# Optimization experiments

Hardware: AMD Instinct MI355X
Metric: run time of the kernel (lower is better)

The kernel has to match this reference:

```python
import jax, jax.numpy as jnp
import numpy as np

B, N, IN_DIM, OUT_DIM, HEADS = 4, 2048, 128, 32, 8
NEG_SLOPE = 0.2


def setup_inputs() -> dict:
    key = jax.random.key(0)
    k_x, k_adj, k_w, k_as, k_ad = jax.random.split(key, 5)
    x = jax.random.normal(k_x, (B, N, IN_DIM), dtype=jnp.float32)
    adj = jax.random.randint(k_adj, (B, N, N), 0, 2).astype(jnp.float32)
    # xavier_uniform bounds
    lim_w = float(np.sqrt(6.0 / (IN_DIM + OUT_DIM)))
    lim_a = float(np.sqrt(6.0 / (OUT_DIM + 1)))
    W = jax.random.uniform(k_w, (HEADS, IN_DIM, OUT_DIM), dtype=jnp.float32, minval=-lim_w, maxval=lim_w)
    a_src = jax.random.uniform(k_as, (HEADS, OUT_DIM), dtype=jnp.float32, minval=-lim_a, maxval=lim_a)
    a_dst = jax.random.uniform(k_ad, (HEADS, OUT_DIM), dtype=jnp.float32, minval=-lim_a, maxval=lim_a)
    return {"x": x, "adj": adj, "W": W, "a_src": a_src, "a_dst": a_dst}


def reference(x, adj, W, a_src, a_dst):
    # Wh: [B,H,N,O]
    Wh = jnp.einsum('bnf,hfo->bhno', x, W)
    alpha_src = jnp.einsum('bhno,ho->bhn', Wh, a_src)  # [B,H,N]
    alpha_dst = jnp.einsum('bhno,ho->bhn', Wh, a_dst)  # [B,H,N]
    # additive scores e[b,h,i,j] = alpha_src[b,h,i] + alpha_dst[b,h,j]
    e = alpha_src[..., :, None] + alpha_dst[..., None, :]
    e = jnp.where(e >= 0, e, NEG_SLOPE * e)  # leaky_relu(0.2)
    n = adj.shape[-1]
    eye = jnp.eye(n, dtype=adj.dtype)
    mask = (adj + eye[None] > 0)[:, None, :, :]  # [B,1,N,N]
    e = jnp.where(mask, e, -jnp.inf)
    attn = jax.nn.softmax(e, axis=-1)  # every row has self-loop -> finite
    out = jnp.einsum('bhij,bhjo->bhio', attn, Wh)  # [B,H,N,O]
    b = x.shape[0]
    out = jnp.transpose(out, (0, 2, 1, 3)).reshape(b, n, HEADS * OUT_DIM)
    return jax.nn.relu(out)
```

## Files before the change

### kernel.cpp

```cpp
#include <hip/hip_runtime.h>
#include <math.h>

#define BB 4
#define NSZ 2048
#define FDIM 128
#define ODIM 32
#define HH 8

typedef short short8 __attribute__((ext_vector_type(8)));
typedef _Float16 half8 __attribute__((ext_vector_type(8)));
typedef float f32x4 __attribute__((ext_vector_type(4)));

#define WS_EAP  0
#define WS_EBP  131072
#define WS_ADJB 262144
#define WS_WHF  786432

__device__ __forceinline__ unsigned hpack(float a, float b) {
    unsigned r;
    asm("v_cvt_pkrtz_f16_f32 %0, %1, %2" : "=v"(r) : "v"(a), "v"(b));
    return r;
}

__global__ __launch_bounds__(256) void k_prep(const float* __restrict__ x,
                                              const float* __restrict__ adj,
                                              const float* __restrict__ W,
                                              const float* __restrict__ a_src,
                                              const float* __restrict__ a_dst,
                                              unsigned* __restrict__ adjb,
                                              int4* __restrict__ whf,
                                              float* __restrict__ eap,
                                              unsigned short* __restrict__ ebe,
                                              unsigned short* __restrict__ ebe2) {
    __shared__ float wsl[FDIM * 33];
    __shared__ unsigned short wlds[64][33];
    int t = threadIdx.x;

    if (blockIdx.x >= 1024) {
        int bid = blockIdx.x - 1024;
#pragma unroll
        for (int it = 0; it < 4; it++) {
            int g = (it * 4096 + bid) * 256 + t;
            int l = g & 7;
            int word = g >> 3;
            int wk = word & 63;
            int row = word >> 6;
            int i = row & (NSZ - 1);
            const float4 v = *(const float4*)&adj[(size_t)row * NSZ + wk * 32 + l * 4];
            unsigned m = 0;
            if (v.x > 0.f) m |= 1u << (l * 4 + 0);
            if (v.y > 0.f) m |= 1u << (l * 4 + 1);
            if (v.z > 0.f) m |= 1u << (l * 4 + 2);
            if (v.w > 0.f) m |= 1u << (l * 4 + 3);
            m |= (unsigned)__shfl_xor((int)m, 1);
            m |= (unsigned)__shfl_xor((int)m, 2);
            m |= (unsigned)__shfl_xor((int)m, 4);
            if (l == 0) {
                int jb = i - wk * 32;
                if (jb >= 0 && jb < 32) m |= 1u << jb;
                adjb[word] = m;
            }
        }
        return;
    }

    int bidx = blockIdx.x;
    int b = bidx >> 8;
    int h = (bidx >> 5) & 7;
    int nt = bidx & 31;
    int n0 = nt * 64;
    int w = t >> 6, lane = t & 63;
    int col = lane & 15, quad = lane >> 4;

#pragma unroll
    for (int m = 0; m < 16; m++) {
        int idx = t + m * 256;
        wsl[(idx >> 5) * 33 + (idx & 31)] = W[(size_t)h * (FDIM * ODIM) + idx];
    }

    const float* xp = x + ((size_t)(b * NSZ) + n0 + w * 16 + col) * FDIM + quad * 8;
    int4 afr[4];
#pragma unroll
    for (int kt = 0; kt < 4; kt++) {
        float4 xa = *(const float4*)(xp + kt * 32);
        float4 xb = *(const float4*)(xp + kt * 32 + 4);
        afr[kt] = make_int4((int)hpack(xa.x, xa.y), (int)hpack(xa.z, xa.w),
                            (int)hpack(xb.x, xb.y), (int)hpack(xb.z, xb.w));
    }
    __syncthreads();

    f32x4 alo = {0.f, 0.f, 0.f, 0.f};
    f32x4 ahi = {0.f, 0.f, 0.f, 0.f};
#pragma unroll
    for (int kt = 0; kt < 4; kt++) {
        half8 a8 = __builtin_bit_cast(half8, afr[kt]);
#pragma unroll
        for (int ot = 0; ot < 2; ot++) {
            unsigned d[4];
#pragma unroll
            for (int jp = 0; jp < 4; jp++) {
                float lo = wsl[(kt * 32 + quad * 8 + 2 * jp) * 33 + ot * 16 + col];
                float hi = wsl[(kt * 32 + quad * 8 + 2 * jp + 1) * 33 + ot * 16 + col];
                d[jp] = hpack(lo, hi);
            }
            int4 bf = make_int4((int)d[0], (int)d[1], (int)d[2], (int)d[3]);
            if (ot == 0)
                alo = __builtin_amdgcn_mfma_f32_16x16x32_f16(a8,
                        __builtin_bit_cast(half8, bf), alo, 0, 0, 0);
            else
                ahi = __builtin_amdgcn_mfma_f32_16x16x32_f16(a8,
                        __builtin_bit_cast(half8, bf), ahi, 0, 0, 0);
        }
    }

    float as0 = a_src[h * ODIM + col], as1 = a_src[h * ODIM + 16 + col];
    float ad0 = a_dst[h * ODIM + col], ad1 = a_dst[h * ODIM + 16 + col];
#pragma unroll
    for (int r = 0; r < 4; r++) {
        float pa = alo[r] * as0 + ahi[r] * as1;
        float pb = alo[r] * ad0 + ahi[r] * ad1;
#pragma unroll
        for (int mk = 1; mk <= 8; mk <<= 1) {
            pa += __shfl_xor(pa, mk);
            pb += __shfl_xor(pb, mk);
        }
        if (col == 0) {
            size_t idx = (size_t)(b * HH + h) * NSZ + n0 + w * 16 + quad * 4 + r;
            eap[idx]  = __expf(-0.8f * pa);
            ebe[idx]  = (unsigned short)(hpack(__expf(pb - 2.f), 0.f) & 0xffffu);
            ebe2[idx] = (unsigned short)(hpack(__expf(0.2f * pb - 2.f), 0.f) & 0xffffu);
        }
    }

#pragma unroll
    for (int r = 0; r < 4; r++) {
        wlds[w * 16 + quad * 4 + r][col]      = (unsigned short)(hpack(alo[r], 0.f) & 0xffffu);
        wlds[w * 16 + quad * 4 + r][col + 16] = (unsigned short)(hpack(ahi[r], 0.f) & 0xffffu);
    }
    __syncthreads();
    int jl = w >> 1, ot = w & 1;
    unsigned d[4];
#pragma unroll
    for (int jp = 0; jp < 4; jp++) {
        unsigned lo = wlds[jl * 32 + quad * 8 + 2 * jp][ot * 16 + col];
        unsigned hi = wlds[jl * 32 + quad * 8 + 2 * jp + 1][ot * 16 + col];
        d[jp] = (hi << 16) | lo;
    }
    int fragid = ((b * HH + h) * 64 + nt * 2 + jl) * 2 + ot;
    whf[(size_t)fragid * 64 + lane] = make_int4((int)d[0], (int)d[1], (int)d[2], (int)d[3]);
}

template<int B>
__device__ __forceinline__ unsigned mexp2(unsigned w, unsigned selhi) {
    unsigned lo, hi, r;
    asm("v_bfe_i32 %0, %1, %2, 1" : "=v"(lo) : "v"(w), "i"(B));
    asm("v_bfe_i32 %0, %1, %2, 1" : "=v"(hi) : "v"(w), "i"(B + 1));
    asm("v_bfi_b32 %0, %1, %2, %3" : "=v"(r) : "s"(selhi), "v"(hi), "v"(lo));
    return r;
}

__device__ __forceinline__ int4 pfrag16(unsigned R2, uint4 e, uint4 g,
                                        unsigned w8, unsigned selhi) {
    unsigned r0, r1, r2, r3, q0, q1, q2, q3;
    asm("v_pk_mul_f16 %0, %1, %2" : "=v"(r0) : "v"(R2), "v"(g.x));
    asm("v_pk_mul_f16 %0, %1, %2" : "=v"(r1) : "v"(R2), "v"(g.y));
    asm("v_pk_mul_f16 %0, %1, %2" : "=v"(r2) : "v"(R2), "v"(g.z));
    asm("v_pk_mul_f16 %0, %1, %2" : "=v"(r3) : "v"(R2), "v"(g.w));
    asm("v_pk_max_f16 %0, %1, %2" : "=v"(q0) : "v"(e.x), "v"(r0));
    asm("v_pk_max_f16 %0, %1, %2" : "=v"(q1) : "v"(e.y), "v"(r1));
    asm("v_pk_max_f16 %0, %1, %2" : "=v"(q2) : "v"(e.z), "v"(r2));
    asm("v_pk_max_f16 %0, %1, %2" : "=v"(q3) : "v"(e.w), "v"(r3));
    return make_int4((int)(q0 & mexp2<0>(w8, selhi)),
                     (int)(q1 & mexp2<2>(w8, selhi)),
                     (int)(q2 & mexp2<4>(w8, selhi)),
                     (int)(q3 & mexp2<6>(w8, selhi)));
}

__global__ __launch_bounds__(256) void k_gat(const int4* __restrict__ whf,
                                             const float* __restrict__ eap,
                                             const unsigned short* __restrict__ ebe,
                                             const unsigned short* __restrict__ ebe2,
                                             const unsigned* __restrict__ adjb,
                                             float* __restrict__ out) {
    __shared__ __align__(16) float smem[2048];
    unsigned short* eble = (unsigned short*)smem;
    unsigned short* eblf = (unsigned short*)smem + 2048;

    int t = threadIdx.x;
    int u = blockIdx.x;
    int unit = (u & 7) * 512 + (u >> 3);
    int b = unit >> 10;
    int h = (unit >> 7) & 7;
    int i0 = (unit & 127) * 16;
    int wave = t >> 6, lane = t & 63;
    int col = lane & 15, quad = lane >> 4, qsh = quad * 8;
    size_t bh = (size_t)(b * HH + h);
    const unsigned selhi = 0xFFFF0000u;

    const float4* ege = (const float4*)(ebe + bh * NSZ);
    const float4* egf = (const float4*)(ebe2 + bh * NSZ);
    ((float4*)eble)[t] = ege[t];
    ((float4*)eblf)[t] = egf[t];

    float R = eap[bh * NSZ + i0 + col];
    unsigned R2 = hpack(R, R);
    const char* mbase = (const char*)(adjb + ((size_t)(b * NSZ) + i0 + col) * 64)
                        + (size_t)wave * 64;
    const int4* bfp = whf + bh * 8192 + (size_t)(wave * 16) * 128 + lane;

    f32x4 a0 = {0.f, 0.f, 0.f, 0.f};
    f32x4 a1 = {0.f, 0.f, 0.f, 0.f};
    f32x4 ad = {0.f, 0.f, 0.f, 0.f};
    const int4 onesv = make_int4(0x3C003C00, 0x3C003C00, 0x3C003C00, 0x3C003C00);
    half8 hones = __builtin_bit_cast(half8, onesv);

    __syncthreads();

    for (int g = 0; g < 4; g++) {
        uint4 m0 = *(const uint4*)(mbase + g * 16);
        int4 blo[4], bhi[4];
#pragma unroll
        for (int q = 0; q < 4; q++) {
            blo[q] = bfp[(g * 4 + q) * 128];
            bhi[q] = bfp[(g * 4 + q) * 128 + 64];
        }
        unsigned ma[4] = {m0.x, m0.y, m0.z, m0.w};
#pragma unroll
        for (int q = 0; q < 4; q++) {
            int jt = wave * 16 + g * 4 + q;
            uint4 ef = *(const uint4*)&eble[jt * 32 + qsh];
            uint4 gf = *(const uint4*)&eblf[jt * 32 + qsh];
            int4 fr = pfrag16(R2, ef, gf, ma[q] >> qsh, selhi);
            half8 af = __builtin_bit_cast(half8, fr);
            half8 b0 = __builtin_bit_cast(half8, blo[q]);
            half8 b1 = __builtin_bit_cast(half8, bhi[q]);
            a0 = __builtin_amdgcn_mfma_f32_16x16x32_f16(af, b0, a0, 0, 0, 0);
            a1 = __builtin_amdgcn_mfma_f32_16x16x32_f16(af, b1, a1, 0, 0, 0);
            ad = __builtin_amdgcn_mfma_f32_16x16x32_f16(af, hones, ad, 0, 0, 0);
        }
    }

    f32x4 (*cb)[3][64] = (f32x4 (*)[3][64])smem;
    __syncthreads();
    if (wave >= 2) {
        cb[wave - 2][0][lane] = a0;
        cb[wave - 2][1][lane] = a1;
        cb[wave - 2][2][lane] = ad;
    }
    __syncthreads();
    if (wave < 2) {
        a0 += cb[wave][0][lane];
        a1 += cb[wave][1][lane];
        ad += cb[wave][2][lane];
    }
    __syncthreads();
    if (wave == 1) {
        cb[0][0][lane] = a0;
        cb[0][1][lane] = a1;
        cb[0][2][lane] = ad;
    }
    __syncthreads();
    if (wave != 0) return;
    a0 += cb[0][0][lane];
    a1 += cb[0][1][lane];
    ad += cb[0][2][lane];

    float* op = out + ((size_t)(b * NSZ) + i0) * (HH * ODIM) + h * ODIM + col;
#pragma unroll
    for (int r = 0; r < 4; r++) {
        int row = quad * 4 + r;
        float inv = 1.0f / ad[r];
        op[(size_t)row * (HH * ODIM)]      = fmaxf(a0[r] * inv, 0.f);
        op[(size_t)row * (HH * ODIM) + 16] = fmaxf(a1[r] * inv, 0.f);
    }
}

extern "C" void kernel_launch(void* const* d_in, const int* in_sizes, int n_in,
                              void* d_out, int out_size, void* d_ws, size_t ws_size,
                              hipStream_t stream) {
    const float* x     = (const float*)d_in[0];
    const float* adj   = (const float*)d_in[1];
    const float* W     = (const float*)d_in[2];
    const float* a_src = (const float*)d_in[3];
    const float* a_dst = (const float*)d_in[4];
    float* out = (float*)d_out;

    float* ws = (float*)d_ws;
    float* eap            = ws + WS_EAP;
    unsigned short* ebe   = (unsigned short*)(ws + WS_EBP);
    unsigned short* ebe2  = (unsigned short*)(ws + WS_EBP + 65536);
    unsigned* adjb        = (unsigned*)(ws + WS_ADJB);
    int4* whf             = (int4*)(ws + WS_WHF);

    k_prep<<<dim3(1024 + 4096), dim3(256), 0, stream>>>(x, adj, W, a_src, a_dst,
                                                        adjb, whf, eap, ebe, ebe2);
    k_gat<<<dim3(BB * HH * (NSZ / 16)), dim3(256), 0, stream>>>(whf, eap, ebe, ebe2, adjb, out);
}
```

Baseline: 133.1 us.

## Process two 16-row tiles per block to reuse Wh and score fragments

Each k_gat block now handles 32 query rows (two 16-row tiles) instead of 16, halving the grid. The Wh B-fragments loaded from global memory and the per-column score values staged in shared memory are reused across both row tiles, which cuts global and LDS traffic per output and amortizes block setup. The cross-wave reduction is reorganized so waves 0 and 1 each finalize one tile and both write outputs. This costs more accumulator registers and shared memory per block and leaves fewer blocks for latency hiding.

```diff
diff --git a/kernel.cpp b/kernel.cpp
--- a/kernel.cpp
+++ b/kernel.cpp
@@ -182,16 +182,16 @@
                                              const unsigned short* __restrict__ ebe2,
                                              const unsigned* __restrict__ adjb,
                                              float* __restrict__ out) {
-    __shared__ __align__(16) float smem[2048];
+    __shared__ __align__(16) float smem[3072];
     unsigned short* eble = (unsigned short*)smem;
     unsigned short* eblf = (unsigned short*)smem + 2048;
 
     int t = threadIdx.x;
     int u = blockIdx.x;
-    int unit = (u & 7) * 512 + (u >> 3);
-    int b = unit >> 10;
-    int h = (unit >> 7) & 7;
-    int i0 = (unit & 127) * 16;
+    int unit = (u & 7) * 256 + (u >> 3);
+    int b = unit >> 9;
+    int h = (unit >> 6) & 7;
+    int i0 = (unit & 63) * 32;
     int wave = t >> 6, lane = t & 63;
     int col = lane & 15, quad = lane >> 4, qsh = quad * 8;
     size_t bh = (size_t)(b * HH + h);
@@ -202,76 +202,91 @@
     ((float4*)eble)[t] = ege[t];
     ((float4*)eblf)[t] = egf[t];
 
-    float R = eap[bh * NSZ + i0 + col];
-    unsigned R2 = hpack(R, R);
+    float Ra = eap[bh * NSZ + i0 + col];
+    float Rb = eap[bh * NSZ + i0 + 16 + col];
+    unsigned R20 = hpack(Ra, Ra);
+    unsigned R21 = hpack(Rb, Rb);
     const char* mbase = (const char*)(adjb + ((size_t)(b * NSZ) + i0 + col) * 64)
                         + (size_t)wave * 64;
     const int4* bfp = whf + bh * 8192 + (size_t)(wave * 16) * 128 + lane;
 
-    f32x4 a0 = {0.f, 0.f, 0.f, 0.f};
-    f32x4 a1 = {0.f, 0.f, 0.f, 0.f};
-    f32x4 ad = {0.f, 0.f, 0.f, 0.f};
+    f32x4 a00 = {0.f,0.f,0.f,0.f}, a01 = {0.f,0.f,0.f,0.f}, a0d = {0.f,0.f,0.f,0.f};
+    f32x4 a10 = {0.f,0.f,0.f,0.f}, a11 = {0.f,0.f,0.f,0.f}, a1d = {0.f,0.f,0.f,0.f};
     const int4 onesv = make_int4(0x3C003C00, 0x3C003C00, 0x3C003C00, 0x3C003C00);
     half8 hones = __builtin_bit_cast(half8, onesv);
 
     __syncthreads();
 
     for (int g = 0; g < 4; g++) {
-        uint4 m0 = *(const uint4*)(mbase + g * 16);
+        uint4 m0 = *(const uint4*)(mbase + 0 * 4096 + g * 16);
+        uint4 m1 = *(const uint4*)(mbase + 1 * 4096 + g * 16);
         int4 blo[4], bhi[4];
 #pragma unroll
         for (int q = 0; q < 4; q++) {
             blo[q] = bfp[(g * 4 + q) * 128];
             bhi[q] = bfp[(g * 4 + q) * 128 + 64];
         }
-        unsigned ma[4] = {m0.x, m0.y, m0.z, m0.w};
+        unsigned ma0[4] = {m0.x, m0.y, m0.z, m0.w};
+        unsigned ma1[4] = {m1.x, m1.y, m1.z, m1.w};
 #pragma unroll
         for (int q = 0; q < 4; q++) {
             int jt = wave * 16 + g * 4 + q;
             uint4 ef = *(const uint4*)&eble[jt * 32 + qsh];
             uint4 gf = *(const uint4*)&eblf[jt * 32 + qsh];
-            int4 fr = pfrag16(R2, ef, gf, ma[q] >> qsh, selhi);
-            half8 af = __builtin_bit_cast(half8, fr);
             half8 b0 = __builtin_bit_cast(half8, blo[q]);
             half8 b1 = __builtin_bit_cast(half8, bhi[q]);
-            a0 = __builtin_amdgcn_mfma_f32_16x16x32_f16(af, b0, a0, 0, 0, 0);
-            a1 = __builtin_amdgcn_mfma_f32_16x16x32_f16(af, b1, a1, 0, 0, 0);
-            ad = __builtin_amdgcn_mfma_f32_16x16x32_f16(af, hones, ad, 0, 0, 0);
+            int4 f0 = pfrag16(R20, ef, gf, ma0[q] >> qsh, selhi);
+            int4 f1 = pfrag16(R21, ef, gf, ma1[q] >> qsh, selhi);
+            half8 af0 = __builtin_bit_cast(half8, f0);
+            half8 af1 = __builtin_bit_cast(half8, f1);
+            a00 = __builtin_amdgcn_mfma_f32_16x16x32_f16(af0, b0, a00, 0, 0, 0);
+            a01 = __builtin_amdgcn_mfma_f32_16x16x32_f16(af0, b1, a01, 0, 0, 0);
+            a0d = __builtin_amdgcn_mfma_f32_16x16x32_f16(af0, hones, a0d, 0, 0, 0);
+            a10 = __builtin_amdgcn_mfma_f32_16x16x32_f16(af1, b0, a10, 0, 0, 0);
+            a11 = __builtin_amdgcn_mfma_f32_16x16x32_f16(af1, b1, a11, 0, 0, 0);
+            a1d = __builtin_amdgcn_mfma_f32_16x16x32_f16(af1, hones, a1d, 0, 0, 0);
         }
     }
 
     f32x4 (*cb)[3][64] = (f32x4 (*)[3][64])smem;
     __syncthreads();
     if (wave >= 2) {
-        cb[wave - 2][0][lane] = a0;
-        cb[wave - 2][1][lane] = a1;
-        cb[wave - 2][2][lane] = ad;
+        int s = (wave - 2) * 2;
+        cb[s][0][lane] = a00;  cb[s][1][lane] = a01;  cb[s][2][lane] = a0d;
+        cb[s + 1][0][lane] = a10;  cb[s + 1][1][lane] = a11;  cb[s + 1][2][lane] = a1d;
     }
     __syncthreads();
     if (wave < 2) {
-        a0 += cb[wave][0][lane];
-        a1 += cb[wave][1][lane];
-        ad += cb[wave][2][lane];
-    }
-    __syncthreads();
-    if (wave == 1) {
-        cb[0][0][lane] = a0;
-        cb[0][1][lane] = a1;
-        cb[0][2][lane] = ad;
-    }
-    __syncthreads();
-    if (wave != 0) return;
-    a0 += cb[0][0][lane];
-    a1 += cb[0][1][lane];
-    ad += cb[0][2][lane];
-
-    float* op = out + ((size_t)(b * NSZ) + i0) * (HH * ODIM) + h * ODIM + col;
+        int s = wave * 2;
+        a00 += cb[s][0][lane];  a01 += cb[s][1][lane];  a0d += cb[s][2][lane];
+        a10 += cb[s + 1][0][lane];  a11 += cb[s + 1][1][lane];  a1d += cb[s + 1][2][lane];
+    }
+    __syncthreads();
+    if (wave == 0) {
+        cb[0][0][lane] = a10;  cb[0][1][lane] = a11;  cb[0][2][lane] = a1d;
+    } else if (wave == 1) {
+        cb[1][0][lane] = a00;  cb[1][1][lane] = a01;  cb[1][2][lane] = a0d;
+    }
+    __syncthreads();
+    if (wave >= 2) return;
+    f32x4 A0, A1, AD;
+    if (wave == 0) {
+        A0 = a00 + cb[1][0][lane];
+        A1 = a01 + cb[1][1][lane];
+        AD = a0d + cb[1][2][lane];
+    } else {
+        A0 = a10 + cb[0][0][lane];
+        A1 = a11 + cb[0][1][lane];
+        AD = a1d + cb[0][2][lane];
+    }
+
+    float* op = out + ((size_t)(b * NSZ) + i0 + wave * 16) * (HH * ODIM) + h * ODIM + col;
 #pragma unroll
     for (int r = 0; r < 4; r++) {
         int row = quad * 4 + r;
-        float inv = 1.0f / ad[r];
-        op[(size_t)row * (HH * ODIM)]      = fmaxf(a0[r] * inv, 0.f);
-        op[(size_t)row * (HH * ODIM) + 16] = fmaxf(a1[r] * inv, 0.f);
+        float inv = 1.0f / AD[r];
+        op[(size_t)row * (HH * ODIM)]      = fmaxf(A0[r] * inv, 0.f);
+        op[(size_t)row * (HH * ODIM) + 16] = fmaxf(A1[r] * inv, 0.f);
     }
 }
 
@@ -294,5 +309,5 @@
 
     k_prep<<<dim3(1024 + 4096), dim3(256), 0, stream>>>(x, adj, W, a_src, a_dst,
                                                         adjb, whf, eap, ebe, ebe2);
-    k_gat<<<dim3(BB * HH * (NSZ / 16)), dim3(256), 0, stream>>>(whf, eap, ebe, ebe2, adjb, out);
-}
+    k_gat<<<dim3(BB * HH * (NSZ / 32)), dim3(256), 0, stream>>>(whf, eap, ebe, ebe2, adjb, out);
+}
```

After: 130.1 us. -2.2%, faster.
